# Optimization experiments

Hardware: AMD Instinct MI355X
Metric: run time of the kernel (lower is better)

Reference implementation:

```python
import jax, jax.numpy as jnp
import numpy as np

N = 50000
E = 600000
F_IN = 128
F_OUT = 128


def setup_inputs() -> dict:
    key = jax.random.key(0)
    k = jax.random.split(key, 8)
    x = jax.random.normal(k[0], (N, F_IN), dtype=jnp.float32)
    edge_index = jax.random.randint(k[1], (2, E), 0, N, dtype=jnp.int64)
    edge_weight = jax.random.uniform(k[2], (E,), dtype=jnp.float32)
    # glorot-initialized linear params (w1 is dead code in the original, kept for faithfulness)
    s = float(np.sqrt(6.0 / (F_IN + F_OUT)))
    W1 = jax.random.uniform(k[3], (F_IN, F_OUT), minval=-s, maxval=s, dtype=jnp.float32)
    b1 = jnp.zeros((F_OUT,), dtype=jnp.float32)
    W2 = jax.random.uniform(k[4], (F_IN, F_OUT), minval=-s, maxval=s, dtype=jnp.float32)
    b2 = jnp.zeros((F_OUT,), dtype=jnp.float32)
    a = jnp.full((1,), 0.5, dtype=jnp.float32)
    b = jnp.full((1,), 0.5, dtype=jnp.float32)
    return {"x": x, "edge_index": edge_index, "edge_weight": edge_weight,
            "W1": W1, "b1": b1, "W2": W2, "b2": b2, "a": a, "b": b}


def reference(x, edge_index, edge_weight, W1, b1, W2, b2, a, b):
    # wh_1 = self.w1(x)  (computed but unused in the original forward)
    wh_1 = x @ W1 + b1  # noqa: F841 (dead, DCE'd under jit)
    src, dst = edge_index[0], edge_index[1]
    # gather neighbor features [E, F_IN], scatter-sum to destination nodes [N, F_IN]
    x_j = jax.ops.segment_sum(x[src], dst, num_segments=N)
    wh_2 = x_j @ W2 + b2
    return wh_2
```

## Files before the change

### kernel.cpp

```cpp
#include <hip/hip_runtime.h>

#define F 128
#define CAP 64
#define LDT 136
#define TR 64
#define KC 32
#define LDA 36
#define LDW 160

typedef __attribute__((ext_vector_type(8))) short bf16x8;
typedef __attribute__((ext_vector_type(4))) float f32x4;

__device__ __forceinline__ unsigned short bf16r(float f)
{
    unsigned u = __float_as_uint(f);
    return (unsigned short)((u + 0x7fffu + ((u >> 16) & 1u)) >> 16);
}

__device__ __forceinline__ unsigned pack2(float a, float b)
{
    return (unsigned)bf16r(a) | ((unsigned)bf16r(b) << 16);
}

__device__ __forceinline__ void load_edge(const int* __restrict__ ei, int is64,
                                          int E, int e, int& s, int& d)
{
    if (is64) {
        s = reinterpret_cast<const int2*>(ei)[e].x;
        d = reinterpret_cast<const int2*>(ei)[(size_t)E + e].x;
    } else {
        s = ei[e];
        d = ei[E + e];
    }
}

__device__ __forceinline__ float4 bf16x4_to_f4(uint2 u)
{
    float4 f;
    f.x = __uint_as_float(u.x << 16);
    f.y = __uint_as_float(u.x & 0xffff0000u);
    f.z = __uint_as_float(u.y << 16);
    f.w = __uint_as_float(u.y & 0xffff0000u);
    return f;
}

__global__ __launch_bounds__(256) void prep_pos_kernel(
    const int* __restrict__ ei, const float* __restrict__ x,
    const float* __restrict__ W, int* __restrict__ cursor,
    unsigned short* __restrict__ csr16, unsigned int* __restrict__ xh,
    unsigned short* __restrict__ Wt, int N, int E, int M4)
{
    const int tid = blockIdx.x * 256 + threadIdx.x;

    if (tid < M4) {
        float4 v = reinterpret_cast<const float4*>(x)[tid];
        uint2 o;
        o.x = pack2(v.x, v.y);
        o.y = pack2(v.z, v.w);
        reinterpret_cast<uint2*>(xh)[tid] = o;
    }
    if (tid < F * F) {
        int k = tid >> 7, n = tid & 127;
        Wt[n * F + k] = bf16r(W[tid]);
    }

    const int base = 4 * tid;
    if (base >= E) return;
    int or_hi = ei[1] | ei[3] | ei[5] | ei[7] | ei[9] | ei[11] | ei[13] | ei[15];
    const int is64 = (or_hi == 0) ? 1 : 0;

    int s[4], d[4];
    int cnt;
    if (base + 3 < E && (E & 3) == 0) {
        cnt = 4;
        if (is64) {
            const int4* sp = reinterpret_cast<const int4*>(ei);
            int4 a = sp[tid * 2], b = sp[tid * 2 + 1];
            s[0] = a.x; s[1] = a.z; s[2] = b.x; s[3] = b.z;
            const int4* dp = reinterpret_cast<const int4*>(ei) + ((size_t)E >> 1);
            int4 c = dp[tid * 2], e4 = dp[tid * 2 + 1];
            d[0] = c.x; d[1] = c.z; d[2] = e4.x; d[3] = e4.z;
        } else {
            int4 sv = reinterpret_cast<const int4*>(ei)[tid];
            int4 dv = reinterpret_cast<const int4*>(ei + E)[tid];
            s[0] = sv.x; s[1] = sv.y; s[2] = sv.z; s[3] = sv.w;
            d[0] = dv.x; d[1] = dv.y; d[2] = dv.z; d[3] = dv.w;
        }
    } else {
        cnt = E - base; if (cnt > 4) cnt = 4;
        for (int j = 0; j < cnt; ++j) load_edge(ei, is64, E, base + j, s[j], d[j]);
        for (int j = cnt; j < 4; ++j) { s[j] = 0; d[j] = 0; }
    }

    int slot[4];
    #pragma unroll
    for (int j = 0; j < 4; ++j)
        slot[j] = (j < cnt) ? atomicAdd(&cursor[d[j]], 1) : CAP;
    #pragma unroll
    for (int j = 0; j < 4; ++j)
        if (slot[j] < CAP) csr16[(size_t)d[j] * CAP + slot[j]] = (unsigned short)s[j];
}

__global__ __launch_bounds__(256) void gather_gemm_kernel(
    const unsigned int* __restrict__ xh, const int* __restrict__ ei,
    const int* __restrict__ cursor, const unsigned short* __restrict__ csr16,
    const unsigned short* __restrict__ Wt, const float* __restrict__ bias,
    float* __restrict__ out, int N, int E)
{
    __shared__ unsigned short sWt[F * LDT];
    __shared__ unsigned short sA[64 * LDT];
    const int t = threadIdx.x;

    const uint4* Wg = reinterpret_cast<const uint4*>(Wt);
    #pragma unroll
    for (int u = 0; u < 8; ++u) {
        int idx = u * 256 + t;
        int n = idx >> 4;
        int c = idx & 15;
        *reinterpret_cast<uint4*>(&sWt[n * LDT + c * 8]) = Wg[idx];
    }

    const int wv = t >> 6, lane = t & 63;
    const int half = lane >> 5, col = lane & 31;
    const int nbase = blockIdx.x * 64 + wv * 16;
    const uint2* x2 = reinterpret_cast<const uint2*>(xh);

    int degl = 0;
    {
        int myn = nbase + (lane & 15);
        if (lane < 16 && myn < N) degl = cursor[myn];
    }

    int node = nbase;
    int deg = __shfl(degl, 0);
    int sv = 0;
    if (node < N && deg <= CAP && lane < deg)
        sv = (int)csr16[(size_t)node * CAP + lane];

    for (int ni = 0; ni < 16; ++ni) {
        int nnode = node + 1;
        int ndeg = (ni < 15) ? __shfl(degl, ni + 1) : 0;
        int nsv = 0;
        if (ni < 15 && nnode < N && ndeg <= CAP && lane < ndeg)
            nsv = (int)csr16[(size_t)nnode * CAP + lane];

        float4 a0 = make_float4(0.f, 0.f, 0.f, 0.f);
        float4 a1 = make_float4(0.f, 0.f, 0.f, 0.f);
        if (node < N) {
            if (deg <= CAP) {
                int i = 0;
                for (; i + 7 < deg; i += 8) {
                    int e0 = __shfl(sv, i + half);
                    int e1 = __shfl(sv, i + 2 + half);
                    int e2 = __shfl(sv, i + 4 + half);
                    int e3 = __shfl(sv, i + 6 + half);
                    float4 v0 = bf16x4_to_f4(x2[(size_t)e0 * 32 + col]);
                    float4 v1 = bf16x4_to_f4(x2[(size_t)e1 * 32 + col]);
                    float4 v2 = bf16x4_to_f4(x2[(size_t)e2 * 32 + col]);
                    float4 v3 = bf16x4_to_f4(x2[(size_t)e3 * 32 + col]);
                    a0.x += v0.x; a0.y += v0.y; a0.z += v0.z; a0.w += v0.w;
                    a1.x += v1.x; a1.y += v1.y; a1.z += v1.z; a1.w += v1.w;
                    a0.x += v2.x; a0.y += v2.y; a0.z += v2.z; a0.w += v2.w;
                    a1.x += v3.x; a1.y += v3.y; a1.z += v3.z; a1.w += v3.w;
                }
                for (; i + 3 < deg; i += 4) {
                    int e0 = __shfl(sv, i + half);
                    int e1 = __shfl(sv, i + 2 + half);
                    float4 v0 = bf16x4_to_f4(x2[(size_t)e0 * 32 + col]);
                    float4 v1 = bf16x4_to_f4(x2[(size_t)e1 * 32 + col]);
                    a0.x += v0.x; a0.y += v0.y; a0.z += v0.z; a0.w += v0.w;
                    a1.x += v1.x; a1.y += v1.y; a1.z += v1.z; a1.w += v1.w;
                }
                for (; i + 1 < deg; i += 2) {
                    int e0 = __shfl(sv, i + half);
                    float4 v0 = bf16x4_to_f4(x2[(size_t)e0 * 32 + col]);
                    a0.x += v0.x; a0.y += v0.y; a0.z += v0.z; a0.w += v0.w;
                }
                if (i < deg) {
                    int e0 = __shfl(sv, i);
                    if (half == 0) {
                        float4 v = bf16x4_to_f4(x2[(size_t)e0 * 32 + col]);
                        a0.x += v.x; a0.y += v.y; a0.z += v.z; a0.w += v.w;
                    }
                }
            } else {
                int or_hi = ei[1] | ei[3] | ei[5] | ei[7] | ei[9] | ei[11] | ei[13] | ei[15];
                int is64 = (or_hi == 0) ? 1 : 0;
                for (int base = 0; base < E; base += 64) {
                    int e = base + lane;
                    int ss = 0, dd = -1;
                    if (e < E) load_edge(ei, is64, E, e, ss, dd);
                    unsigned long long m = __ballot(dd == node);
                    while (m) {
                        int i = __ffsll((long long)m) - 1;
                        m &= m - 1;
                        int sb = __shfl(ss, i);
                        float4 v = bf16x4_to_f4(x2[(size_t)sb * 32 + col]);
                        if (half == 0) { a0.x += v.x; a0.y += v.y; a0.z += v.z; a0.w += v.w; }
                    }
                }
            }
        }
        a0.x += a1.x; a0.y += a1.y; a0.z += a1.z; a0.w += a1.w;
        a0.x += __shfl_xor(a0.x, 32);
        a0.y += __shfl_xor(a0.y, 32);
        a0.z += __shfl_xor(a0.z, 32);
        a0.w += __shfl_xor(a0.w, 32);
        if (half == 0) {
            uint2 o;
            o.x = pack2(a0.x, a0.y);
            o.y = pack2(a0.z, a0.w);
            *reinterpret_cast<uint2*>(&sA[(wv * 16 + ni) * LDT + col * 4]) = o;
        }
        node = nnode; deg = ndeg; sv = nsv;
    }

    __syncthreads();

    const int quad = lane >> 4, n15 = lane & 15;
    f32x4 acc[8];
    #pragma unroll
    for (int i = 0; i < 8; ++i) acc[i] = (f32x4){0.f, 0.f, 0.f, 0.f};

    #pragma unroll
    for (int kc = 0; kc < F; kc += 32) {
        bf16x8 af = *reinterpret_cast<const bf16x8*>(
            &sA[(wv * 16 + n15) * LDT + kc + quad * 8]);
        #pragma unroll
        for (int nt = 0; nt < 8; ++nt) {
            bf16x8 bfr = *reinterpret_cast<const bf16x8*>(
                &sWt[(nt * 16 + n15) * LDT + kc + quad * 8]);
            acc[nt] = __builtin_amdgcn_mfma_f32_16x16x32_bf16(af, bfr, acc[nt], 0, 0, 0);
        }
    }

    const int rbase = blockIdx.x * 64 + wv * 16;
    #pragma unroll
    for (int nt = 0; nt < 8; ++nt) {
        float bv = bias[nt * 16 + n15];
        #pragma unroll
        for (int reg = 0; reg < 4; ++reg) {
            int row = rbase + quad * 4 + reg;
            if (row < N)
                out[(size_t)row * F + nt * 16 + n15] = acc[nt][reg] + bv;
        }
    }
}

__global__ __launch_bounds__(256) void init_kernel(
    const int* __restrict__ ei, int* __restrict__ flag,
    int* __restrict__ zero_arr, int N)
{
    int i = blockIdx.x * 256 + threadIdx.x;
    if (i < N) zero_arr[i] = 0;
    if (i == 0) {
        int or_hi = ei[1] | ei[3] | ei[5] | ei[7] | ei[9] | ei[11] | ei[13] | ei[15];
        *flag = (or_hi == 0) ? 1 : 0;
    }
}

__global__ __launch_bounds__(256) void position_bucket_kernel(
    const int* __restrict__ ei, const int* __restrict__ flag_p,
    int* __restrict__ cursor, int* __restrict__ csr_src, int E)
{
    int e = blockIdx.x * 256 + threadIdx.x;
    if (e >= E) return;
    int s, d;
    load_edge(ei, *flag_p, E, e, s, d);
    int slot = atomicAdd(&cursor[d], 1);
    if (slot < CAP) csr_src[(size_t)d * CAP + slot] = s;
}

__global__ __launch_bounds__(256) void gather_bucket_f32_kernel(
    const float* __restrict__ x, const int* __restrict__ ei,
    const int* __restrict__ flag_p, const int* __restrict__ cursor,
    const int* __restrict__ csr_src, float* __restrict__ agg, int N, int E)
{
    int node = blockIdx.x * 4 + (threadIdx.x >> 6);
    if (node >= N) return;
    int lane = threadIdx.x & 63;
    int half = lane >> 5;
    int col = lane & 31;
    int deg = cursor[node];

    const float4* x4 = reinterpret_cast<const float4*>(x);
    float4 a0 = make_float4(0.f, 0.f, 0.f, 0.f);
    float4 a1 = make_float4(0.f, 0.f, 0.f, 0.f);

    if (deg <= CAP) {
        int sv = (lane < deg) ? csr_src[(size_t)node * CAP + lane] : 0;
        int i = 0;
        for (; i + 3 < deg; i += 4) {
            int e0 = __shfl(sv, i + half);
            int e1 = __shfl(sv, i + 2 + half);
            float4 v0 = x4[(size_t)e0 * 32 + col];
            float4 v1 = x4[(size_t)e1 * 32 + col];
            a0.x += v0.x; a0.y += v0.y; a0.z += v0.z; a0.w += v0.w;
            a1.x += v1.x; a1.y += v1.y; a1.z += v1.z; a1.w += v1.w;
        }
        for (; i + 1 < deg; i += 2) {
            int e0 = __shfl(sv, i + half);
            float4 v0 = x4[(size_t)e0 * 32 + col];
            a0.x += v0.x; a0.y += v0.y; a0.z += v0.z; a0.w += v0.w;
        }
        if (i < deg) {
            int e0 = __shfl(sv, i);
            if (half == 0) {
                float4 v = x4[(size_t)e0 * 32 + col];
                a0.x += v.x; a0.y += v.y; a0.z += v.z; a0.w += v.w;
            }
        }
    } else {
        int is64 = *flag_p;
        for (int base = 0; base < E; base += 64) {
            int e = base + lane;
            int s = 0, d = -1;
            if (e < E) load_edge(ei, is64, E, e, s, d);
            unsigned long long m = __ballot(d == node);
            while (m) {
                int i = __ffsll((long long)m) - 1;
                m &= m - 1;
                int sb = __shfl(s, i);
                float4 v = x4[(size_t)sb * 32 + col];
                if (half == 0) { a0.x += v.x; a0.y += v.y; a0.z += v.z; a0.w += v.w; }
            }
        }
    }
    a0.x += a1.x; a0.y += a1.y; a0.z += a1.z; a0.w += a1.w;
    a0.x += __shfl_xor(a0.x, 32);
    a0.y += __shfl_xor(a0.y, 32);
    a0.z += __shfl_xor(a0.z, 32);
    a0.w += __shfl_xor(a0.w, 32);
    if (half == 0)
        reinterpret_cast<float4*>(agg)[(size_t)node * 32 + col] = a0;
}

__global__ __launch_bounds__(256) void scatter_kernel(
    const float* __restrict__ x, const int* __restrict__ ei,
    const int* __restrict__ flag_p, float* __restrict__ agg, int E)
{
    int tid = blockIdx.x * 256 + threadIdx.x;
    int e = tid >> 5;
    if (e >= E) return;
    int c = (tid & 31) << 2;
    int s, d;
    load_edge(ei, *flag_p, E, e, s, d);
    float4 v = *reinterpret_cast<const float4*>(x + (size_t)s * F + c);
    float* o = agg + (size_t)d * F + c;
    unsafeAtomicAdd(o + 0, v.x);
    unsafeAtomicAdd(o + 1, v.y);
    unsafeAtomicAdd(o + 2, v.z);
    unsafeAtomicAdd(o + 3, v.w);
}

__global__ __launch_bounds__(256) void gemm_kernel(
    float* __restrict__ io, const float* __restrict__ W,
    const float* __restrict__ bias, int N)
{
    __shared__ float sA[TR * LDA];
    __shared__ float sW[KC * LDW];
    const int t = threadIdx.x;
    const int row0 = blockIdx.x * TR;
    const int g = t & 7;
    const int r = t >> 3;

    float acc[2][16];
    #pragma unroll
    for (int i = 0; i < 2; ++i)
        #pragma unroll
        for (int j = 0; j < 16; ++j) acc[i][j] = 0.0f;

    for (int kc = 0; kc < F; kc += KC) {
        #pragma unroll
        for (int u = 0; u < 2; ++u) {
            int idx = u * 256 + t;
            int row = idx >> 3;
            int k4 = (idx & 7) * 4;
            int grow = row0 + row;
            float4 v = (grow < N)
                ? *reinterpret_cast<const float4*>(io + (size_t)grow * F + kc + k4)
                : make_float4(0.f, 0.f, 0.f, 0.f);
            *reinterpret_cast<float4*>(&sA[row * LDA + k4]) = v;
        }
        #pragma unroll
        for (int u = 0; u < 4; ++u) {
            int idx = u * 256 + t;
            int kk = idx >> 5;
            int f4 = (idx & 31) * 4;
            float4 v = *reinterpret_cast<const float4*>(W + (size_t)(kc + kk) * F + f4);
            int chunk = f4 >> 4;
            int within = f4 & 15;
            *reinterpret_cast<float4*>(&sW[kk * LDW + chunk * 20 + within]) = v;
        }
        __syncthreads();

        #pragma unroll 8
        for (int kk = 0; kk < KC; ++kk) {
            const float* wp = &sW[kk * LDW + g * 20];
            const float4 w0 = *reinterpret_cast<const float4*>(wp + 0);
            const float4 w1 = *reinterpret_cast<const float4*>(wp + 4);
            const float4 w2 = *reinterpret_cast<const float4*>(wp + 8);
            const float4 w3 = *reinterpret_cast<const float4*>(wp + 12);
            #pragma unroll
            for (int i = 0; i < 2; ++i) {
                const float xv = sA[(r * 2 + i) * LDA + kk];
                acc[i][0]  += xv * w0.x;  acc[i][1]  += xv * w0.y;
                acc[i][2]  += xv * w0.z;  acc[i][3]  += xv * w0.w;
                acc[i][4]  += xv * w1.x;  acc[i][5]  += xv * w1.y;
                acc[i][6]  += xv * w1.z;  acc[i][7]  += xv * w1.w;
                acc[i][8]  += xv * w2.x;  acc[i][9]  += xv * w2.y;
                acc[i][10] += xv * w2.z;  acc[i][11] += xv * w2.w;
                acc[i][12] += xv * w3.x;  acc[i][13] += xv * w3.y;
                acc[i][14] += xv * w3.z;  acc[i][15] += xv * w3.w;
            }
        }
        __syncthreads();
    }

    float bv[16];
    #pragma unroll
    for (int j = 0; j < 16; ++j) bv[j] = bias[g * 16 + j];
    #pragma unroll
    for (int i = 0; i < 2; ++i) {
        int row = row0 + r * 2 + i;
        if (row < N) {
            float* o = io + (size_t)row * F + g * 16;
            #pragma unroll
            for (int j4 = 0; j4 < 4; ++j4) {
                float4 v;
                v.x = acc[i][j4 * 4 + 0] + bv[j4 * 4 + 0];
                v.y = acc[i][j4 * 4 + 1] + bv[j4 * 4 + 1];
                v.z = acc[i][j4 * 4 + 2] + bv[j4 * 4 + 2];
                v.w = acc[i][j4 * 4 + 3] + bv[j4 * 4 + 3];
                *reinterpret_cast<float4*>(o + j4 * 4) = v;
            }
        }
    }
}

static inline size_t al16(size_t v) { return (v + 15) & ~(size_t)15; }

extern "C" void kernel_launch(void* const* d_in, const int* in_sizes, int n_in,
                              void* d_out, int out_size, void* d_ws, size_t ws_size,
                              hipStream_t stream) {
    const float* x  = (const float*)d_in[0];
    const int*   ei = (const int*)d_in[1];
    const float* W2 = (const float*)d_in[5];
    const float* b2 = (const float*)d_in[6];
    float* out = (float*)d_out;

    const int N = in_sizes[0] / F;
    const int E = in_sizes[2];
    const int nblk = (N + 255) / 256;
    const int eblk = (E + 255) / 256;

    char* wsb = (char*)d_ws;
    size_t off = 64;
    int* cursor = (int*)(wsb + off);
    off = al16(off + (size_t)N * 4);
    unsigned short* csr16 = (unsigned short*)(wsb + off);
    off = al16(off + (size_t)N * CAP * 2);
    unsigned int* xh = (unsigned int*)(wsb + off);
    off = al16(off + (size_t)N * (F / 2) * 4);
    unsigned short* Wt = (unsigned short*)(wsb + off);
    off += (size_t)F * F * 2;
    size_t needA = off;

    size_t needB = (size_t)(16 + N + (size_t)N * CAP) * sizeof(int);

    if (ws_size >= needA && N <= 65536) {
        hipMemsetAsync(cursor, 0, (size_t)N * sizeof(int), stream);

        const int M4 = N * (F / 4);
        int gp = (M4 + 255) / 256;
        int ge = (((E + 3) / 4) + 255) / 256; if (ge > gp) gp = ge;
        int gw = (F * F + 255) / 256;         if (gw > gp) gp = gw;
        prep_pos_kernel<<<gp, 256, 0, stream>>>(
            ei, x, W2, cursor, csr16, xh, Wt, N, E, M4);

        gather_gemm_kernel<<<(N + 63) / 64, 256, 0, stream>>>(
            xh, ei, cursor, csr16, Wt, b2, out, N, E);
    } else if (ws_size >= needB) {
        int* flag    = (int*)wsb;
        int* curs    = flag + 16;
        int* csr_src = curs + N;
        init_kernel<<<nblk, 256, 0, stream>>>(ei, flag, curs, N);
        position_bucket_kernel<<<eblk, 256, 0, stream>>>(ei, flag, curs, csr_src, E);
        gather_bucket_f32_kernel<<<(N + 3) / 4, 256, 0, stream>>>(
            x, ei, flag, curs, csr_src, out, N, E);
        gemm_kernel<<<(N + TR - 1) / TR, 256, 0, stream>>>(out, W2, b2, N);
    } else {
        int* flag = (int*)wsb;
        init_kernel<<<1, 64, 0, stream>>>(ei, flag, flag + 16, 0);
        hipMemsetAsync(out, 0, (size_t)N * F * sizeof(float), stream);
        scatter_kernel<<<(E * 32 + 255) / 256, 256, 0, stream>>>(x, ei, flag, out, E);
        gemm_kernel<<<(N + TR - 1) / TR, 256, 0, stream>>>(out, W2, b2, N);
    }
}
```

Before: 194.4 us.

## Use single-wave blocks with async global-to-LDS gathers and direct W reads

Replaces the 256-thread gather+GEMM kernel with 64-thread blocks that each handle 16 nodes. Neighbor rows are now fetched with global_load_lds async copies into an LDS staging buffer, four edges at a time with 16-byte loads per lane. The W tile is no longer staged in shared memory; MFMA operands are read straight from global (L2-resident) memory. This cuts LDS footprint and removes the block barrier, aiming for more resident waves and wider loads. The cost is a full vmcnt wait per chunk, serializing load and accumulate, plus redundant global W reads in every block.

```diff
diff --git a/kernel.cpp b/kernel.cpp
--- a/kernel.cpp
+++ b/kernel.cpp
@@ -44,6 +44,14 @@
     return f;
 }
 
+__device__ __forceinline__ void async_copy16(const void* g, void* lds)
+{
+    __builtin_amdgcn_global_load_lds(
+        (const __attribute__((address_space(1))) unsigned int*)g,
+        (__attribute__((address_space(3))) unsigned int*)lds,
+        16, 0, 0);
+}
+
 __global__ __launch_bounds__(256) void prep_pos_kernel(
     const int* __restrict__ ei, const float* __restrict__ x,
     const float* __restrict__ W, int* __restrict__ cursor,
@@ -66,7 +74,11 @@
 
     const int base = 4 * tid;
     if (base >= E) return;
-    int or_hi = ei[1] | ei[3] | ei[5] | ei[7] | ei[9] | ei[11] | ei[13] | ei[15];
+    int or_hi = 0;
+    {
+        int lim = 2 * E; if (lim > 16) lim = 16;
+        for (int j = 1; j < lim; j += 2) or_hi |= ei[j];
+    }
     const int is64 = (or_hi == 0) ? 1 : 0;
 
     int s[4], d[4];
@@ -101,91 +113,75 @@
         if (slot[j] < CAP) csr16[(size_t)d[j] * CAP + slot[j]] = (unsigned short)s[j];
 }
 
-__global__ __launch_bounds__(256) void gather_gemm_kernel(
+__global__ __launch_bounds__(64, 4) void gather_gemm64_kernel(
     const unsigned int* __restrict__ xh, const int* __restrict__ ei,
     const int* __restrict__ cursor, const unsigned short* __restrict__ csr16,
     const unsigned short* __restrict__ Wt, const float* __restrict__ bias,
     float* __restrict__ out, int N, int E)
 {
-    __shared__ unsigned short sWt[F * LDT];
-    __shared__ unsigned short sA[64 * LDT];
-    const int t = threadIdx.x;
-
-    const uint4* Wg = reinterpret_cast<const uint4*>(Wt);
-    #pragma unroll
-    for (int u = 0; u < 8; ++u) {
-        int idx = u * 256 + t;
-        int n = idx >> 4;
-        int c = idx & 15;
-        *reinterpret_cast<uint4*>(&sWt[n * LDT + c * 8]) = Wg[idx];
-    }
-
-    const int wv = t >> 6, lane = t & 63;
-    const int half = lane >> 5, col = lane & 31;
-    const int nbase = blockIdx.x * 64 + wv * 16;
-    const uint2* x2 = reinterpret_cast<const uint2*>(xh);
+    __shared__ __align__(16) char stg[4096];
+    __shared__ __align__(16) unsigned short sA[16][LDT];
+    const int lane = threadIdx.x;
+    const int eg = lane >> 4;
+    const int c  = lane & 15;
+    const int nbase = blockIdx.x * 16;
 
     int degl = 0;
-    {
-        int myn = nbase + (lane & 15);
-        if (lane < 16 && myn < N) degl = cursor[myn];
-    }
-
-    int node = nbase;
+    if (lane < 16 && nbase + lane < N) degl = cursor[nbase + lane];
+
     int deg = __shfl(degl, 0);
     int sv = 0;
-    if (node < N && deg <= CAP && lane < deg)
-        sv = (int)csr16[(size_t)node * CAP + lane];
+    if (nbase < N) sv = (int)csr16[(size_t)nbase * CAP + lane];
 
     for (int ni = 0; ni < 16; ++ni) {
-        int nnode = node + 1;
+        const int node = nbase + ni;
+        const int nnode = node + 1;
         int ndeg = (ni < 15) ? __shfl(degl, ni + 1) : 0;
         int nsv = 0;
-        if (ni < 15 && nnode < N && ndeg <= CAP && lane < ndeg)
+        if (ni < 15 && nnode < N)
             nsv = (int)csr16[(size_t)nnode * CAP + lane];
 
-        float4 a0 = make_float4(0.f, 0.f, 0.f, 0.f);
-        float4 a1 = make_float4(0.f, 0.f, 0.f, 0.f);
+        float f[8];
+        #pragma unroll
+        for (int j = 0; j < 8; ++j) f[j] = 0.f;
+
         if (node < N) {
             if (deg <= CAP) {
-                int i = 0;
-                for (; i + 7 < deg; i += 8) {
-                    int e0 = __shfl(sv, i + half);
-                    int e1 = __shfl(sv, i + 2 + half);
-                    int e2 = __shfl(sv, i + 4 + half);
-                    int e3 = __shfl(sv, i + 6 + half);
-                    float4 v0 = bf16x4_to_f4(x2[(size_t)e0 * 32 + col]);
-                    float4 v1 = bf16x4_to_f4(x2[(size_t)e1 * 32 + col]);
-                    float4 v2 = bf16x4_to_f4(x2[(size_t)e2 * 32 + col]);
-                    float4 v3 = bf16x4_to_f4(x2[(size_t)e3 * 32 + col]);
-                    a0.x += v0.x; a0.y += v0.y; a0.z += v0.z; a0.w += v0.w;
-                    a1.x += v1.x; a1.y += v1.y; a1.z += v1.z; a1.w += v1.w;
-                    a0.x += v2.x; a0.y += v2.y; a0.z += v2.z; a0.w += v2.w;
-                    a1.x += v3.x; a1.y += v3.y; a1.z += v3.z; a1.w += v3.w;
-                }
-                for (; i + 3 < deg; i += 4) {
-                    int e0 = __shfl(sv, i + half);
-                    int e1 = __shfl(sv, i + 2 + half);
-                    float4 v0 = bf16x4_to_f4(x2[(size_t)e0 * 32 + col]);
-                    float4 v1 = bf16x4_to_f4(x2[(size_t)e1 * 32 + col]);
-                    a0.x += v0.x; a0.y += v0.y; a0.z += v0.z; a0.w += v0.w;
-                    a1.x += v1.x; a1.y += v1.y; a1.z += v1.z; a1.w += v1.w;
-                }
-                for (; i + 1 < deg; i += 2) {
-                    int e0 = __shfl(sv, i + half);
-                    float4 v0 = bf16x4_to_f4(x2[(size_t)e0 * 32 + col]);
-                    a0.x += v0.x; a0.y += v0.y; a0.z += v0.z; a0.w += v0.w;
-                }
-                if (i < deg) {
-                    int e0 = __shfl(sv, i);
-                    if (half == 0) {
-                        float4 v = bf16x4_to_f4(x2[(size_t)e0 * 32 + col]);
-                        a0.x += v.x; a0.y += v.y; a0.z += v.z; a0.w += v.w;
+                for (int ch = 0; ch < deg; ch += 16) {
+                    int nE = deg - ch; if (nE > 16) nE = 16;
+                    int nL = (nE + 3) >> 2;
+                    asm volatile("s_waitcnt lgkmcnt(0)" ::: "memory");
+                    __builtin_amdgcn_sched_barrier(0);
+                    for (int l = 0; l < nL; ++l) {
+                        int e = ch + l * 4 + eg;
+                        int esel = (e < deg) ? e : (deg - 1);
+                        int src = __shfl(sv, esel);
+                        async_copy16((const char*)xh + ((size_t)src * 256 + (size_t)c * 16),
+                                     stg + l * 1024);
+                    }
+                    asm volatile("s_waitcnt vmcnt(0)" ::: "memory");
+                    __builtin_amdgcn_sched_barrier(0);
+                    for (int l = 0; l < nL; ++l) {
+                        uint4 v = *reinterpret_cast<const uint4*>(stg + l * 1024 + lane * 16);
+                        if (ch + l * 4 + eg < deg) {
+                            f[0] += __uint_as_float(v.x << 16);
+                            f[1] += __uint_as_float(v.x & 0xffff0000u);
+                            f[2] += __uint_as_float(v.y << 16);
+                            f[3] += __uint_as_float(v.y & 0xffff0000u);
+                            f[4] += __uint_as_float(v.z << 16);
+                            f[5] += __uint_as_float(v.z & 0xffff0000u);
+                            f[6] += __uint_as_float(v.w << 16);
+                            f[7] += __uint_as_float(v.w & 0xffff0000u);
+                        }
                     }
                 }
             } else {
-                int or_hi = ei[1] | ei[3] | ei[5] | ei[7] | ei[9] | ei[11] | ei[13] | ei[15];
-                int is64 = (or_hi == 0) ? 1 : 0;
+                int or_hi = 0;
+                {
+                    int lim = 2 * E; if (lim > 16) lim = 16;
+                    for (int j = 1; j < lim; j += 2) or_hi |= ei[j];
+                }
+                const int is64 = (or_hi == 0) ? 1 : 0;
                 for (int base = 0; base < E; base += 64) {
                     int e = base + lane;
                     int ss = 0, dd = -1;
@@ -195,27 +191,36 @@
                         int i = __ffsll((long long)m) - 1;
                         m &= m - 1;
                         int sb = __shfl(ss, i);
-                        float4 v = bf16x4_to_f4(x2[(size_t)sb * 32 + col]);
-                        if (half == 0) { a0.x += v.x; a0.y += v.y; a0.z += v.z; a0.w += v.w; }
+                        if (eg == 0) {
+                            uint4 v = reinterpret_cast<const uint4*>(xh)[(size_t)sb * 16 + c];
+                            f[0] += __uint_as_float(v.x << 16);
+                            f[1] += __uint_as_float(v.x & 0xffff0000u);
+                            f[2] += __uint_as_float(v.y << 16);
+                            f[3] += __uint_as_float(v.y & 0xffff0000u);
+                            f[4] += __uint_as_float(v.z << 16);
+                            f[5] += __uint_as_float(v.z & 0xffff0000u);
+                            f[6] += __uint_as_float(v.w << 16);
+                            f[7] += __uint_as_float(v.w & 0xffff0000u);
+                        }
                     }
                 }
             }
         }
-        a0.x += a1.x; a0.y += a1.y; a0.z += a1.z; a0.w += a1.w;
-        a0.x += __shfl_xor(a0.x, 32);
-        a0.y += __shfl_xor(a0.y, 32);
-        a0.z += __shfl_xor(a0.z, 32);
-        a0.w += __shfl_xor(a0.w, 32);
-        if (half == 0) {
-            uint2 o;
-            o.x = pack2(a0.x, a0.y);
-            o.y = pack2(a0.z, a0.w);
-            *reinterpret_cast<uint2*>(&sA[(wv * 16 + ni) * LDT + col * 4]) = o;
-        }
-        node = nnode; deg = ndeg; sv = nsv;
-    }
-
-    __syncthreads();
+        #pragma unroll
+        for (int j = 0; j < 8; ++j) {
+            f[j] += __shfl_xor(f[j], 16);
+            f[j] += __shfl_xor(f[j], 32);
+        }
+        if (eg == 0) {
+            uint4 o;
+            o.x = pack2(f[0], f[1]);
+            o.y = pack2(f[2], f[3]);
+            o.z = pack2(f[4], f[5]);
+            o.w = pack2(f[6], f[7]);
+            *reinterpret_cast<uint4*>(&sA[ni][c * 8]) = o;
+        }
+        deg = ndeg; sv = nsv;
+    }
 
     const int quad = lane >> 4, n15 = lane & 15;
     f32x4 acc[8];
@@ -224,23 +229,21 @@
 
     #pragma unroll
     for (int kc = 0; kc < F; kc += 32) {
-        bf16x8 af = *reinterpret_cast<const bf16x8*>(
-            &sA[(wv * 16 + n15) * LDT + kc + quad * 8]);
+        bf16x8 af = *reinterpret_cast<const bf16x8*>(&sA[n15][kc + quad * 8]);
         #pragma unroll
         for (int nt = 0; nt < 8; ++nt) {
             bf16x8 bfr = *reinterpret_cast<const bf16x8*>(
-                &sWt[(nt * 16 + n15) * LDT + kc + quad * 8]);
+                Wt + (size_t)(nt * 16 + n15) * F + kc + quad * 8);
             acc[nt] = __builtin_amdgcn_mfma_f32_16x16x32_bf16(af, bfr, acc[nt], 0, 0, 0);
         }
     }
 
-    const int rbase = blockIdx.x * 64 + wv * 16;
     #pragma unroll
     for (int nt = 0; nt < 8; ++nt) {
         float bv = bias[nt * 16 + n15];
         #pragma unroll
         for (int reg = 0; reg < 4; ++reg) {
-            int row = rbase + quad * 4 + reg;
+            int row = nbase + quad * 4 + reg;
             if (row < N)
                 out[(size_t)row * F + nt * 16 + n15] = acc[nt][reg] + bv;
         }
@@ -452,6 +455,7 @@
     const int N = in_sizes[0] / F;
     const int E = in_sizes[2];
     const int nblk = (N + 255) / 256;
+    const int M4 = N * (F / 4);
     const int eblk = (E + 255) / 256;
 
     char* wsb = (char*)d_ws;
@@ -471,14 +475,13 @@
     if (ws_size >= needA && N <= 65536) {
         hipMemsetAsync(cursor, 0, (size_t)N * sizeof(int), stream);
 
-        const int M4 = N * (F / 4);
         int gp = (M4 + 255) / 256;
         int ge = (((E + 3) / 4) + 255) / 256; if (ge > gp) gp = ge;
         int gw = (F * F + 255) / 256;         if (gw > gp) gp = gw;
         prep_pos_kernel<<<gp, 256, 0, stream>>>(
             ei, x, W2, cursor, csr16, xh, Wt, N, E, M4);
 
-        gather_gemm_kernel<<<(N + 63) / 64, 256, 0, stream>>>(
+        gather_gemm64_kernel<<<(N + 15) / 16, 64, 0, stream>>>(
             xh, ei, cursor, csr16, Wt, b2, out, N, E);
     } else if (ws_size >= needB) {
         int* flag    = (int*)wsb;
```

New measurement: 168.8 us. 1.15x faster.
